# Kernel tuning notes

Hardware: AMD Instinct MI355X
Metric: run time of the kernel (lower is better)

Reference implementation:

```python
import jax, jax.numpy as jnp
import numpy as np

B, L, C, D = 32, 256, 16, 128
WORD_VOCAB, CHR_VOCAB = 50000, 128


def conv1d(x, w, b):
    # x: [N, D, T], w: [D_out, D_in, 3], torch Conv1d (cross-correlation), padding=1
    y = jax.lax.conv_general_dilated(x, w, window_strides=(1,), padding=[(1, 1)],
                                     dimension_numbers=('NCH', 'OIH', 'NCH'))
    return y + b[None, :, None]


def setup_inputs() -> dict:
    key = jax.random.key(0)
    k1, k2, k3, k4, k5, k6, k7, k8 = jax.random.split(key, 8)
    word_vector = jax.random.randint(k1, (B, L), 0, WORD_VOCAB)
    words_in_char = jax.random.randint(k2, (B, L, C), 0, CHR_VOCAB)
    # embedding tables, padding_idx=0 -> row 0 is zeros
    word_table = (jax.random.normal(k3, (WORD_VOCAB, D), jnp.float32) * 0.02).at[0].set(0.0)
    chr_table = (jax.random.normal(k4, (CHR_VOCAB, D), jnp.float32) * 0.02).at[0].set(0.0)
    scale = 1.0 / np.sqrt(D * 3)
    conv_chr_w = jax.random.normal(k5, (D, D, 3), jnp.float32) * scale
    conv_chr_b = jax.random.normal(k6, (D,), jnp.float32) * scale
    conv_word_w = jax.random.normal(k7, (D, D, 3), jnp.float32) * scale
    conv_word_b = jax.random.normal(k8, (D,), jnp.float32) * scale
    return dict(word_vector=word_vector, words_in_char=words_in_char,
                word_table=word_table, chr_table=chr_table,
                conv_chr_w=conv_chr_w, conv_chr_b=conv_chr_b,
                conv_word_w=conv_word_w, conv_word_b=conv_word_b)


def reference(word_vector, words_in_char, word_table, chr_table,
              conv_chr_w, conv_chr_b, conv_word_w, conv_word_b):
    # --- char path (batched version of the per-word Python loop) ---
    chr_emb = chr_table[words_in_char]                       # [B, L, C, D]
    x = chr_emb.reshape(B * L, C, D).transpose(0, 2, 1)      # [B*L, D, C]
    word_conv = conv1d(x, conv_chr_w, conv_chr_b)            # [B*L, D, C]
    char_feats = word_conv.max(axis=2).reshape(B, L, D)      # max over char positions
    # --- word path ---
    word_emb = word_table[word_vector]                       # [B, L, D]
    out = conv1d(word_emb.transpose(0, 2, 1), conv_word_w, conv_word_b)  # [B, D, L]
    # stack both branch outputs into one array: [2, B, D, L]
    return jnp.stack([out, char_feats.transpose(0, 2, 1)])
```

## Files before the change

kernel.cpp:

```cpp
#include <hip/hip_runtime.h>

typedef __attribute__((ext_vector_type(8))) short short8;
typedef __attribute__((ext_vector_type(4))) float float4_t;

#define NB 32
#define NL 256
#define ND 128
#define OUT_PLANE (NB * ND * NL)
#define XS 136
#define FR_WORD 49152
#define CHRB 98304

__device__ inline unsigned short f2bf(float f) {
    union { float f; unsigned int i; } c;
    c.f = f;
    unsigned int r = c.i + 0x7FFFu + ((c.i >> 16) & 1u);
    return (unsigned short)(r >> 16);
}

__global__ void make_frags(const float* __restrict__ Wc,
                           const float* __restrict__ Ww,
                           const float* __restrict__ chrT,
                           unsigned short* __restrict__ out) {
    int i = blockIdx.x * 256 + threadIdx.x;
    if (i < CHRB) {
        const float* W = (i < FR_WORD) ? Wc : Ww;
        int ii = (i < FR_WORD) ? i : i - FR_WORD;
        int j    = ii & 7;
        int lane = (ii >> 3) & 63;
        int nt   = (ii >> 9) & 7;
        int s    = ii >> 12;
        int dout = nt * 16 + (lane & 15);
        int t    = s >> 2;
        int k    = (s & 3) * 32 + ((lane >> 4) & 3) * 8 + j;
        out[i] = f2bf(W[(dout * 128 + k) * 3 + t]);
    } else {
        int j = i - CHRB;
        out[i] = f2bf(chrT[j]);
    }
}

__global__ __launch_bounds__(128, 2) void conv_kernel(
    const int* __restrict__ wv, const int* __restrict__ wic,
    const float* __restrict__ wordT,
    const unsigned short* __restrict__ ws,
    const float* __restrict__ biasC, const float* __restrict__ biasW,
    float* __restrict__ out) {
    __shared__ unsigned short X[2][18 * XS];
    const int tid  = threadIdx.x;
    const int wave = tid >> 6, lane = tid & 63;
    const int m = lane & 15, quad = lane >> 4;
    const int bid = blockIdx.x;

    if (bid >= 512) {
        const unsigned short* chrB = ws + CHRB;
        const int w0 = (bid - 512) * 8;
        const int b = w0 >> 8, l0 = w0 & 255;
        short8 bfrag[12][4];
#pragma unroll
        for (int s = 0; s < 12; ++s)
#pragma unroll
            for (int p = 0; p < 4; ++p)
                bfrag[s][p] = *(const short8*)(
                    ws + (((s * 8 + wave * 4 + p) * 64 + lane) << 3));
        float bb[4];
#pragma unroll
        for (int p = 0; p < 4; ++p) bb[p] = biasC[wave * 64 + p * 16 + m];

        for (int p = tid; p < XS; p += 128) {
            X[0][p] = 0; X[0][17 * XS + p] = 0;
            X[1][p] = 0; X[1][17 * XS + p] = 0;
        }
        const int ra = tid >> 4, sub = tid & 15;

        {
            int j0 = wic[w0 * 16 + ra];
            int j1 = wic[w0 * 16 + ra + 8];
            short8 g0 = *(const short8*)(chrB + j0 * 128 + sub * 8);
            short8 g1 = *(const short8*)(chrB + j1 * 128 + sub * 8);
            *(short8*)&X[0][(ra + 1) * XS + sub * 8] = g0;
            *(short8*)&X[0][(ra + 9) * XS + sub * 8] = g1;
        }
        int iA0 = wic[(w0 + 1) * 16 + ra];
        int iA1 = wic[(w0 + 1) * 16 + ra + 8];
        __syncthreads();

        float v[4][4];
#pragma unroll
        for (int wl = 0; wl < 8; ++wl) {
            const int cur = wl & 1;
            short8 g0, g1;
            if (wl < 7) {
                g0 = *(const short8*)(chrB + iA0 * 128 + sub * 8);
                g1 = *(const short8*)(chrB + iA1 * 128 + sub * 8);
            }
            int iB0 = 0, iB1 = 0;
            if (wl < 6) {
                iB0 = wic[(w0 + wl + 2) * 16 + ra];
                iB1 = wic[(w0 + wl + 2) * 16 + ra + 8];
            }

            float4_t acc[4];
#pragma unroll
            for (int p = 0; p < 4; ++p) acc[p] = (float4_t){0.f, 0.f, 0.f, 0.f};
#pragma unroll
            for (int s = 0; s < 12; ++s) {
                short8 a = *(const short8*)&X[cur][(m + (s >> 2)) * XS +
                                                  (s & 3) * 32 + quad * 8];
#pragma unroll
                for (int p = 0; p < 4; ++p)
                    acc[p] = __builtin_amdgcn_mfma_f32_16x16x32_bf16(
                        a, bfrag[s][p], acc[p], 0, 0, 0);
            }

            if (wl < 7) {
                *(short8*)&X[cur ^ 1][(ra + 1) * XS + sub * 8] = g0;
                *(short8*)&X[cur ^ 1][(ra + 9) * XS + sub * 8] = g1;
                iA0 = iB0; iA1 = iB1;
            }
            __syncthreads();

#pragma unroll
            for (int p = 0; p < 4; ++p) {
                float t = fmaxf(fmaxf(acc[p].x, acc[p].y),
                                fmaxf(acc[p].z, acc[p].w));
                t = fmaxf(t, __shfl_xor(t, 16, 64));
                t = fmaxf(t, __shfl_xor(t, 32, 64));
                v[p][wl & 3] = t + bb[p];
            }
            if ((wl & 3) == 3 && quad == 0) {
                float* obase = out + OUT_PLANE + b * (ND * NL) + l0 + (wl & 4);
#pragma unroll
                for (int p = 0; p < 4; ++p) {
                    float4_t pk = {v[p][0], v[p][1], v[p][2], v[p][3]};
                    *(float4_t*)&obase[(wave * 64 + p * 16 + m) * NL] = pk;
                }
            }
        }
    } else {
        const int b = bid >> 4, l0 = (bid & 15) << 4;
        short8 bfrag[12][4];
#pragma unroll
        for (int s = 0; s < 12; ++s)
#pragma unroll
            for (int p = 0; p < 4; ++p)
                bfrag[s][p] = *(const short8*)(
                    ws + FR_WORD + (((s * 8 + wave * 4 + p) * 64 + lane) << 3));
        float bb[4];
#pragma unroll
        for (int p = 0; p < 4; ++p) bb[p] = biasW[wave * 64 + p * 16 + m];

#pragma unroll
        for (int i0 = 0; i0 < 2; ++i0) {
            int i = tid + i0 * 128;
            if (i < 144) {
                int rr = i >> 3, sg = i & 7;
                int l = l0 + rr - 1;
                int idx = (l >= 0 && l < NL) ? wv[b * NL + l] : 0;
                const float4_t* src =
                    (const float4_t*)(wordT + idx * 128 + sg * 16);
                float4_t f0 = src[0], f1 = src[1], f2 = src[2], f3 = src[3];
                unsigned short t16[16];
                t16[0]=f2bf(f0.x); t16[1]=f2bf(f0.y); t16[2]=f2bf(f0.z); t16[3]=f2bf(f0.w);
                t16[4]=f2bf(f1.x); t16[5]=f2bf(f1.y); t16[6]=f2bf(f1.z); t16[7]=f2bf(f1.w);
                t16[8]=f2bf(f2.x); t16[9]=f2bf(f2.y); t16[10]=f2bf(f2.z); t16[11]=f2bf(f2.w);
                t16[12]=f2bf(f3.x); t16[13]=f2bf(f3.y); t16[14]=f2bf(f3.z); t16[15]=f2bf(f3.w);
                *(short8*)&X[0][rr * XS + sg * 16]     = *(const short8*)&t16[0];
                *(short8*)&X[0][rr * XS + sg * 16 + 8] = *(const short8*)&t16[8];
            }
        }
        __syncthreads();

        float4_t acc[4];
#pragma unroll
        for (int p = 0; p < 4; ++p) acc[p] = (float4_t){0.f, 0.f, 0.f, 0.f};
#pragma unroll
        for (int s = 0; s < 12; ++s) {
            short8 a = *(const short8*)&X[0][(m + (s >> 2)) * XS +
                                            (s & 3) * 32 + quad * 8];
#pragma unroll
            for (int p = 0; p < 4; ++p)
                acc[p] = __builtin_amdgcn_mfma_f32_16x16x32_bf16(
                    a, bfrag[s][p], acc[p], 0, 0, 0);
        }

        float* obase = out + b * (ND * NL) + l0 + quad * 4;
#pragma unroll
        for (int p = 0; p < 4; ++p) {
            int dout = wave * 64 + p * 16 + m;
            float4_t pk;
            pk.x = acc[p].x + bb[p];
            pk.y = acc[p].y + bb[p];
            pk.z = acc[p].z + bb[p];
            pk.w = acc[p].w + bb[p];
            *(float4_t*)&obase[dout * NL] = pk;
        }
    }
}

extern "C" void kernel_launch(void* const* d_in, const int* in_sizes, int n_in,
                              void* d_out, int out_size, void* d_ws,
                              size_t ws_size, hipStream_t stream) {
    const int* word_vector   = (const int*)d_in[0];
    const int* words_in_char = (const int*)d_in[1];
    const float* word_table  = (const float*)d_in[2];
    const float* chr_table   = (const float*)d_in[3];
    const float* conv_chr_w  = (const float*)d_in[4];
    const float* conv_chr_b  = (const float*)d_in[5];
    const float* conv_word_w = (const float*)d_in[6];
    const float* conv_word_b = (const float*)d_in[7];
    float* out            = (float*)d_out;
    unsigned short* wsp   = (unsigned short*)d_ws;

    make_frags<<<448, 256, 0, stream>>>(conv_chr_w, conv_word_w, chr_table, wsp);
    conv_kernel<<<1536, 128, 0, stream>>>(word_vector, words_in_char,
                                          word_table, wsp,
                                          conv_chr_b, conv_word_b, out);
}
```

Before: 107.6 us.

## Quad-buffer char-path LDS and process two words per barrier

```diff
diff --git a/kernel.cpp b/kernel.cpp
--- a/kernel.cpp
+++ b/kernel.cpp
@@ -40,13 +40,29 @@
     }
 }
 
+__device__ __forceinline__ void mfma12(const unsigned short* __restrict__ buf,
+                                       const short8 bfrag[12][4],
+                                       int m, int quad, float4_t acc[4]) {
+#pragma unroll
+    for (int p = 0; p < 4; ++p) acc[p] = (float4_t){0.f, 0.f, 0.f, 0.f};
+#pragma unroll
+    for (int s = 0; s < 12; ++s) {
+        short8 a = *(const short8*)&buf[(m + (s >> 2)) * XS +
+                                        (s & 3) * 32 + quad * 8];
+#pragma unroll
+        for (int p = 0; p < 4; ++p)
+            acc[p] = __builtin_amdgcn_mfma_f32_16x16x32_bf16(
+                a, bfrag[s][p], acc[p], 0, 0, 0);
+    }
+}
+
 __global__ __launch_bounds__(128, 2) void conv_kernel(
     const int* __restrict__ wv, const int* __restrict__ wic,
     const float* __restrict__ wordT,
     const unsigned short* __restrict__ ws,
     const float* __restrict__ biasC, const float* __restrict__ biasW,
     float* __restrict__ out) {
-    __shared__ unsigned short X[2][18 * XS];
+    __shared__ unsigned short X[4][18 * XS];
     const int tid  = threadIdx.x;
     const int wave = tid >> 6, lane = tid & 63;
     const int m = lane & 15, quad = lane >> 4;
@@ -67,58 +83,52 @@
 #pragma unroll
         for (int p = 0; p < 4; ++p) bb[p] = biasC[wave * 64 + p * 16 + m];
 
-        for (int p = tid; p < XS; p += 128) {
-            X[0][p] = 0; X[0][17 * XS + p] = 0;
-            X[1][p] = 0; X[1][17 * XS + p] = 0;
-        }
+        for (int p = tid; p < XS; p += 128)
+#pragma unroll
+            for (int q = 0; q < 4; ++q) { X[q][p] = 0; X[q][17 * XS + p] = 0; }
+
         const int ra = tid >> 4, sub = tid & 15;
 
-        {
-            int j0 = wic[w0 * 16 + ra];
-            int j1 = wic[w0 * 16 + ra + 8];
+#pragma unroll
+        for (int q = 0; q < 2; ++q) {
+            int j0 = wic[(w0 + q) * 16 + ra];
+            int j1 = wic[(w0 + q) * 16 + ra + 8];
             short8 g0 = *(const short8*)(chrB + j0 * 128 + sub * 8);
             short8 g1 = *(const short8*)(chrB + j1 * 128 + sub * 8);
-            *(short8*)&X[0][(ra + 1) * XS + sub * 8] = g0;
-            *(short8*)&X[0][(ra + 9) * XS + sub * 8] = g1;
-        }
-        int iA0 = wic[(w0 + 1) * 16 + ra];
-        int iA1 = wic[(w0 + 1) * 16 + ra + 8];
+            *(short8*)&X[q][(ra + 1) * XS + sub * 8] = g0;
+            *(short8*)&X[q][(ra + 9) * XS + sub * 8] = g1;
+        }
+        int iA0 = wic[(w0 + 2) * 16 + ra];
+        int iA1 = wic[(w0 + 2) * 16 + ra + 8];
+        int iC0 = wic[(w0 + 3) * 16 + ra];
+        int iC1 = wic[(w0 + 3) * 16 + ra + 8];
         __syncthreads();
 
         float v[4][4];
 #pragma unroll
-        for (int wl = 0; wl < 8; ++wl) {
-            const int cur = wl & 1;
+        for (int j = 0; j < 8; j += 2) {
             short8 g0, g1;
-            if (wl < 7) {
+            if (j < 6) {
                 g0 = *(const short8*)(chrB + iA0 * 128 + sub * 8);
                 g1 = *(const short8*)(chrB + iA1 * 128 + sub * 8);
             }
-            int iB0 = 0, iB1 = 0;
-            if (wl < 6) {
-                iB0 = wic[(w0 + wl + 2) * 16 + ra];
-                iB1 = wic[(w0 + wl + 2) * 16 + ra + 8];
-            }
 
             float4_t acc[4];
-#pragma unroll
-            for (int p = 0; p < 4; ++p) acc[p] = (float4_t){0.f, 0.f, 0.f, 0.f};
-#pragma unroll
-            for (int s = 0; s < 12; ++s) {
-                short8 a = *(const short8*)&X[cur][(m + (s >> 2)) * XS +
-                                                  (s & 3) * 32 + quad * 8];
-#pragma unroll
-                for (int p = 0; p < 4; ++p)
-                    acc[p] = __builtin_amdgcn_mfma_f32_16x16x32_bf16(
-                        a, bfrag[s][p], acc[p], 0, 0, 0);
-            }
-
-            if (wl < 7) {
-                *(short8*)&X[cur ^ 1][(ra + 1) * XS + sub * 8] = g0;
-                *(short8*)&X[cur ^ 1][(ra + 9) * XS + sub * 8] = g1;
-                iA0 = iB0; iA1 = iB1;
-            }
-            __syncthreads();
+            mfma12(X[j & 3], bfrag, m, quad, acc);
+
+            short8 h0, h1;
+            if (j < 6) {
+                *(short8*)&X[(j + 2) & 3][(ra + 1) * XS + sub * 8] = g0;
+                *(short8*)&X[(j + 2) & 3][(ra + 9) * XS + sub * 8] = g1;
+                h0 = *(const short8*)(chrB + iC0 * 128 + sub * 8);
+                h1 = *(const short8*)(chrB + iC1 * 128 + sub * 8);
+                if (j < 4) {
+                    iA0 = wic[(w0 + j + 4) * 16 + ra];
+                    iA1 = wic[(w0 + j + 4) * 16 + ra + 8];
+                    iC0 = wic[(w0 + j + 5) * 16 + ra];
+                    iC1 = wic[(w0 + j + 5) * 16 + ra + 8];
+                }
+            }
 
 #pragma unroll
             for (int p = 0; p < 4; ++p) {
@@ -126,16 +136,33 @@
                                 fmaxf(acc[p].z, acc[p].w));
                 t = fmaxf(t, __shfl_xor(t, 16, 64));
                 t = fmaxf(t, __shfl_xor(t, 32, 64));
-                v[p][wl & 3] = t + bb[p];
-            }
-            if ((wl & 3) == 3 && quad == 0) {
-                float* obase = out + OUT_PLANE + b * (ND * NL) + l0 + (wl & 4);
+                v[p][j & 3] = t + bb[p];
+            }
+
+            mfma12(X[(j + 1) & 3], bfrag, m, quad, acc);
+
+            if (j < 6) {
+                *(short8*)&X[(j + 3) & 3][(ra + 1) * XS + sub * 8] = h0;
+                *(short8*)&X[(j + 3) & 3][(ra + 9) * XS + sub * 8] = h1;
+            }
+
+#pragma unroll
+            for (int p = 0; p < 4; ++p) {
+                float t = fmaxf(fmaxf(acc[p].x, acc[p].y),
+                                fmaxf(acc[p].z, acc[p].w));
+                t = fmaxf(t, __shfl_xor(t, 16, 64));
+                t = fmaxf(t, __shfl_xor(t, 32, 64));
+                v[p][(j + 1) & 3] = t + bb[p];
+            }
+            if (((j + 1) & 3) == 3 && quad == 0) {
+                float* obase = out + OUT_PLANE + b * (ND * NL) + l0 + (j & 4);
 #pragma unroll
                 for (int p = 0; p < 4; ++p) {
                     float4_t pk = {v[p][0], v[p][1], v[p][2], v[p][3]};
                     *(float4_t*)&obase[(wave * 64 + p * 16 + m) * NL] = pk;
                 }
             }
+            __syncthreads();
         }
     } else {
         const int b = bid >> 4, l0 = (bid & 15) << 4;
```

Result: no change. 106.2 us (-1.4%).
